# Kernel optimization log

Measured on AMD Instinct MI355X. Metric: run time of the kernel, lower is better.

## Reference

```python
import jax, jax.numpy as jnp
import numpy as np

HEADS = 4
DIM_HEAD = 32
GROUPS = 32  # min(256//4, 32)
EPS = 1e-5


def setup_inputs() -> dict:
    key = jax.random.key(0)
    ks = jax.random.split(key, 5)
    B, C, H, W = 16, 256, 64, 64
    CD, HC, WC = 512, 32, 32
    hid = HEADS * DIM_HEAD  # 128
    return {
        "x": jax.random.normal(ks[0], (B, C, H, W), jnp.float32),
        "cond": jax.random.normal(ks[1], (B, CD, HC, WC), jnp.float32),
        "gn_w": jnp.ones((C,), jnp.float32),
        "gn_b": jnp.zeros((C,), jnp.float32),
        "w_q": jax.random.normal(ks[2], (hid, C), jnp.float32) * 0.05,
        "b_q": jnp.zeros((hid,), jnp.float32),
        "w_kv": jax.random.normal(ks[3], (2 * hid, CD), jnp.float32) * 0.05,
        "b_kv": jnp.zeros((2 * hid,), jnp.float32),
        "w_out": jax.random.normal(ks[4], (C, hid), jnp.float32) * 0.05,
        "b_out": jnp.zeros((C,), jnp.float32),
    }


def _group_norm(x, w, b):
    # x: (B, C, H, W); normalize per group over (channels-in-group, H, W)
    B, C, H, W = x.shape
    xg = x.reshape(B, GROUPS, C // GROUPS, H, W)
    mu = jnp.mean(xg, axis=(2, 3, 4), keepdims=True)
    var = jnp.var(xg, axis=(2, 3, 4), keepdims=True)
    xn = ((xg - mu) * jax.lax.rsqrt(var + EPS)).reshape(B, C, H, W)
    return xn * w[None, :, None, None] + b[None, :, None, None]


def _conv1x1(x, w, b):
    # x: (B, Cin, H, W), w: (Cout, Cin), b: (Cout,)
    return jnp.einsum('oc,bchw->bohw', w, x) + b[None, :, None, None]


def reference(x, cond, gn_w, gn_b, w_q, b_q, w_kv, b_kv, w_out, b_out):
    B, C, H, W = x.shape
    hid = HEADS * DIM_HEAD
    xn = _group_norm(x, gn_w, gn_b)
    q = _conv1x1(xn, w_q, b_q)          # (B, hid, H, W)
    kv = _conv1x1(cond, w_kv, b_kv)     # (B, 2*hid, Hc, Wc)
    Nc = kv.shape[2] * kv.shape[3]
    N = H * W
    k = kv[:, :hid].reshape(B, HEADS, DIM_HEAD, Nc)
    v = kv[:, hid:].reshape(B, HEADS, DIM_HEAD, Nc)
    q = q.reshape(B, HEADS, DIM_HEAD, N)
    k = jax.nn.softmax(k, axis=-1)
    # kv outer product: (B, heads, d, e)
    context = jnp.einsum('bhdn,bhen->bhde', k, v)
    # query contraction over d: (B, heads, e, n)
    out = jnp.einsum('bhde,bhdn->bhen', context, q)
    out = out.reshape(B, hid, H, W)
    return _conv1x1(out, w_out, b_out)
```

## Files before the change

### kernel.cpp

```cpp
#include <hip/hip_runtime.h>
#include <hip/hip_bf16.h>

typedef __attribute__((ext_vector_type(8))) short bf16x8;
typedef __attribute__((ext_vector_type(4))) float f32x4;

__device__ __forceinline__ ushort f2bf(float f) {
    __hip_bfloat16 h = __float2bfloat16(f);
    return __builtin_bit_cast(ushort, h);
}
__device__ __forceinline__ float bflo(unsigned u) { return __uint_as_float(u << 16); }
__device__ __forceinline__ float bfhi(unsigned u) { return __uint_as_float(u & 0xffff0000u); }

__device__ __forceinline__ void unpack8(uint4 r, float* o) {
    o[0] = bflo(r.x); o[1] = bfhi(r.x); o[2] = bflo(r.y); o[3] = bfhi(r.y);
    o[4] = bflo(r.z); o[5] = bfhi(r.z); o[6] = bflo(r.w); o[7] = bfhi(r.w);
}

__global__ __launch_bounds__(256) void prep_kernel(const float* __restrict__ w,
                                                   ushort* __restrict__ o,
                                                   float* __restrict__ zbase,
                                                   const float* __restrict__ x,
                                                   float* __restrict__ statacc) {
    __shared__ float red[8];
    int bid = blockIdx.x, t = threadIdx.x;
    if (bid < 512) {
        int i = bid * 256 + t;
        if (i < 67584) zbase[i] = 0.f;
        o[i] = f2bf(w[i]);
    } else {
        int bg = bid - 512;
        const float4* xp = (const float4*)(x + (size_t)bg * 32768);
        float s = 0.f, ss = 0.f;
        #pragma unroll
        for (int j = 0; j < 32; ++j) {
            float4 v = xp[t + 256 * j];
            s  += v.x + v.y + v.z + v.w;
            ss += v.x*v.x + v.y*v.y + v.z*v.z + v.w*v.w;
        }
        #pragma unroll
        for (int off = 32; off > 0; off >>= 1) {
            s  += __shfl_down(s, off, 64);
            ss += __shfl_down(ss, off, 64);
        }
        int wave = t >> 6;
        if ((t & 63) == 0) { red[wave * 2] = s; red[wave * 2 + 1] = ss; }
        __syncthreads();
        if (t == 0) {
            statacc[bg * 2]     = red[0] + red[2] + red[4] + red[6];
            statacc[bg * 2 + 1] = red[1] + red[3] + red[5] + red[7];
        }
    }
}

__global__ __launch_bounds__(256) void kv_gemm(const ushort* __restrict__ wkv16,
                                               const float* __restrict__ cond,
                                               const float* __restrict__ b_kv,
                                               ushort* __restrict__ kv16) {
    __shared__ ushort lA[128 * 64];
    __shared__ ushort lB[64 * 64];
    __shared__ float scratch[64 * 64];
    int nb = blockIdx.x, ob = blockIdx.y, b = blockIdx.z;
    int col0 = nb * 64, row0 = ob * 128;
    int t = threadIdx.x;
    int l = t & 63, wid = t >> 6;
    int wr = wid >> 1, wc = wid & 1;
    int lr = l & 15, lg = l >> 4;
    const ushort* Ab = wkv16 + (size_t)row0 * 512;
    const float* Bb = cond + (size_t)b * 512 * 1024 + col0;
    int sp = t & 31, sj = t >> 5;
    int rA_ = t >> 3;
    int gA_ = (t & 7) ^ (rA_ & 7);
    int rB = t >> 4, gB = t & 15;
    uint4 a0_, a1_, a2_, a3_;
    float4 b0_, b1_, b2_, b3_;
    float4 c0_, c1_, c2_, c3_;
#define KG_LOADA(k0) { \
    a0_ = *(const uint4*)(Ab + (size_t)(rA_)      * 512 + (k0) + gA_ * 8); \
    a1_ = *(const uint4*)(Ab + (size_t)(32 + rA_) * 512 + (k0) + gA_ * 8); \
    a2_ = *(const uint4*)(Ab + (size_t)(64 + rA_) * 512 + (k0) + gA_ * 8); \
    a3_ = *(const uint4*)(Ab + (size_t)(96 + rA_) * 512 + (k0) + gA_ * 8); }
#define KG_LOADB0(k0) { \
    b0_ = *(const float4*)&Bb[(size_t)((k0) + rB)      * 1024 + gB * 4]; \
    b1_ = *(const float4*)&Bb[(size_t)((k0) + 16 + rB) * 1024 + gB * 4]; \
    b2_ = *(const float4*)&Bb[(size_t)((k0) + 32 + rB) * 1024 + gB * 4]; \
    b3_ = *(const float4*)&Bb[(size_t)((k0) + 48 + rB) * 1024 + gB * 4]; }
#define KG_LOADB1(k0) { \
    c0_ = *(const float4*)&Bb[(size_t)((k0) + rB)      * 1024 + gB * 4]; \
    c1_ = *(const float4*)&Bb[(size_t)((k0) + 16 + rB) * 1024 + gB * 4]; \
    c2_ = *(const float4*)&Bb[(size_t)((k0) + 32 + rB) * 1024 + gB * 4]; \
    c3_ = *(const float4*)&Bb[(size_t)((k0) + 48 + rB) * 1024 + gB * 4]; }
#define KG_WRITEA() { \
    *(uint4*)((char*)lA + (size_t)(t) * 16)       = a0_; \
    *(uint4*)((char*)lA + (size_t)(256 + t) * 16) = a1_; \
    *(uint4*)((char*)lA + (size_t)(512 + t) * 16) = a2_; \
    *(uint4*)((char*)lA + (size_t)(768 + t) * 16) = a3_; }
#define KG_WRITEB(v0, v1, v2, v3) { \
    *(float4*)((char*)scratch + (rB)      * 256 + (gB ^ (((rB)      >> 1) & 15)) * 16) = v0; \
    *(float4*)((char*)scratch + (16 + rB) * 256 + (gB ^ (((16 + rB) >> 1) & 15)) * 16) = v1; \
    *(float4*)((char*)scratch + (32 + rB) * 256 + (gB ^ (((32 + rB) >> 1) & 15)) * 16) = v2; \
    *(float4*)((char*)scratch + (48 + rB) * 256 + (gB ^ (((48 + rB) >> 1) & 15)) * 16) = v3; }
#define KG_PACK() { \
    int swz = sp & 15; \
    float4 s0 = *(const float4*)((char*)scratch + (2*sp)   * 256 + ((2*sj)   ^ swz) * 16); \
    float4 s1 = *(const float4*)((char*)scratch + (2*sp)   * 256 + ((2*sj+1) ^ swz) * 16); \
    float4 s2 = *(const float4*)((char*)scratch + (2*sp+1) * 256 + ((2*sj)   ^ swz) * 16); \
    float4 s3 = *(const float4*)((char*)scratch + (2*sp+1) * 256 + ((2*sj+1) ^ swz) * 16); \
    float c0v[8] = {s0.x, s0.y, s0.z, s0.w, s1.x, s1.y, s1.z, s1.w}; \
    float c1v[8] = {s2.x, s2.y, s2.z, s2.w, s3.x, s3.y, s3.z, s3.w}; \
    _Pragma("unroll") \
    for (int w = 0; w < 8; ++w) { \
        int n = sj * 8 + w; \
        unsigned pk = (unsigned)f2bf(c0v[w]) | ((unsigned)f2bf(c1v[w]) << 16); \
        *(unsigned*)((char*)lB + n * 128 + (((sp >> 2) ^ (n & 7)) * 16) + (sp & 3) * 4) = pk; \
    } }
#define KG_MFMA() { \
    _Pragma("unroll") \
    for (int ks = 0; ks < 2; ++ks) { \
        bf16x8 av[4], bv[2]; \
        _Pragma("unroll") \
        for (int mi = 0; mi < 4; ++mi) { \
            int ar = wr * 64 + mi * 16 + lr; \
            int q = (ks * 4 + lg) ^ (ar & 7); \
            av[mi] = *(const bf16x8*)((const char*)lA + ar * 128 + q * 16); \
        } \
        _Pragma("unroll") \
        for (int ni = 0; ni < 2; ++ni) { \
            int br = wc * 32 + ni * 16 + lr; \
            int q = (ks * 4 + lg) ^ (br & 7); \
            bv[ni] = *(const bf16x8*)((const char*)lB + br * 128 + q * 16); \
        } \
        _Pragma("unroll") \
        for (int mi = 0; mi < 4; ++mi) \
            _Pragma("unroll") \
            for (int ni = 0; ni < 2; ++ni) \
                acc[mi][ni] = __builtin_amdgcn_mfma_f32_16x16x32_bf16( \
                    av[mi], bv[ni], acc[mi][ni], 0, 0, 0); \
    } }
    KG_LOADA(0); KG_LOADB0(0); KG_LOADB1(64);
    f32x4 acc[4][2] = {};
    #pragma unroll
    for (int ii = 0; ii < 4; ++ii) {
        int k0 = ii * 128;
        KG_WRITEA();
        KG_WRITEB(b0_, b1_, b2_, b3_);
        __syncthreads();
        KG_LOADA(k0 + 64);
        if (ii < 3) KG_LOADB0(k0 + 128);
        KG_PACK();
        __syncthreads();
        KG_MFMA();
        __syncthreads();
        KG_WRITEA();
        KG_WRITEB(c0_, c1_, c2_, c3_);
        __syncthreads();
        if (ii < 3) { KG_LOADA(k0 + 128); KG_LOADB1(k0 + 192); }
        KG_PACK();
        __syncthreads();
        KG_MFMA();
        __syncthreads();
    }
#undef KG_LOADA
#undef KG_LOADB0
#undef KG_LOADB1
#undef KG_WRITEA
#undef KG_WRITEB
#undef KG_PACK
#undef KG_MFMA
    int orow = row0 + wr * 64, ocol = col0 + wc * 32 + lr;
    #pragma unroll
    for (int mi = 0; mi < 4; ++mi) {
        int rb = orow + mi * 16 + lg * 4;
        float4 b4 = *(const float4*)&b_kv[rb];
        float bvr[4] = {b4.x, b4.y, b4.z, b4.w};
        #pragma unroll
        for (int ni = 0; ni < 2; ++ni) {
            int cc = ocol + ni * 16;
            #pragma unroll
            for (int r = 0; r < 4; ++r)
                kv16[((size_t)b * 256 + rb + r) * 1024 + cc] = f2bf(acc[mi][ni][r] + bvr[r]);
        }
    }
}

__global__ __launch_bounds__(256) void ctx_partial_kernel(const ushort* __restrict__ kv,
                                                          float* __restrict__ rowsum,
                                                          float* __restrict__ ctx) {
    int bh = blockIdx.y, b = bh >> 2, h = bh & 3;
    int n0 = blockIdx.x * 128;
    __shared__ float pl[32][129], vl[32][129];
    int t = threadIdx.x;
    int r = t >> 3, cs = (t & 7) * 16;
    const ushort* kp = kv + ((size_t)b * 256 + h * 32 + r) * 1024 + n0 + cs;
    const ushort* vp = kv + ((size_t)b * 256 + 128 + h * 32 + r) * 1024 + n0 + cs;
    float kvals[16], vvals[16];
    unpack8(((const uint4*)kp)[0], kvals);
    unpack8(((const uint4*)kp)[1], kvals + 8);
    unpack8(((const uint4*)vp)[0], vvals);
    unpack8(((const uint4*)vp)[1], vvals + 8);
    float psum = 0.f;
    #pragma unroll
    for (int i = 0; i < 16; ++i) {
        float e = __expf(kvals[i]);
        pl[r][cs + i] = e;
        vl[r][cs + i] = vvals[i];
        psum += e;
    }
    psum += __shfl_xor(psum, 1, 64);
    psum += __shfl_xor(psum, 2, 64);
    psum += __shfl_xor(psum, 4, 64);
    if ((t & 7) == 0) atomicAdd(&rowsum[bh * 32 + r], psum);
    __syncthreads();
    int d0 = t >> 5, e0 = t & 31;
    float acc[4] = {0.f, 0.f, 0.f, 0.f};
    #pragma unroll 8
    for (int nn = 0; nn < 128; ++nn) {
        float vv = vl[e0][nn];
        #pragma unroll
        for (int i = 0; i < 4; ++i)
            acc[i] += pl[d0 + 8 * i][nn] * vv;
    }
    #pragma unroll
    for (int i = 0; i < 4; ++i)
        atomicAdd(&ctx[((size_t)bh * 32 + d0 + 8 * i) * 32 + e0], acc[i]);
}

__global__ __launch_bounds__(256) void a_kernel(const float* __restrict__ ctx,
                                                const float* __restrict__ rowsum,
                                                const float* __restrict__ w_out,
                                                const float* __restrict__ w_q,
                                                const float* __restrict__ b_q,
                                                const float* __restrict__ statacc,
                                                const float* __restrict__ gn_w,
                                                const float* __restrict__ gn_b,
                                                const float* __restrict__ b_out,
                                                ushort* __restrict__ A16,
                                                float* __restrict__ biasb) {
    __shared__ float ctxl[4][32][33];
    __shared__ float wol[16][128];
    __shared__ float ml[16][128];
    __shared__ float cbuf[256][17];
    __shared__ float pbuf[16][17];
    int b = blockIdx.x >> 4, ot = (blockIdx.x & 15) << 4;
    int t = threadIdx.x;
    #pragma unroll
    for (int j = 0; j < 16; ++j) {
        int e = t + 256 * j;
        float inv = 1.f / rowsum[b * 128 + (e >> 5)];
        ctxl[e >> 10][(e >> 5) & 31][e & 31] = ctx[(size_t)b * 4096 + e] * inv;
    }
    #pragma unroll
    for (int j = 0; j < 8; ++j) {
        int e = t + 256 * j;
        wol[e >> 7][e & 127] = w_out[(ot + (e >> 7)) * 128 + (e & 127)];
    }
    __syncthreads();
    #pragma unroll
    for (int j = 0; j < 8; ++j) {
        int e = t + 256 * j;
        int o = e >> 7, hd = e & 127, h = hd >> 5, d = hd & 31;
        float acc = 0.f;
        #pragma unroll
        for (int ee = 0; ee < 32; ++ee) acc += wol[o][h * 32 + ee] * ctxl[h][d][ee];
        ml[o][hd] = acc;
    }
    __syncthreads();
    int c = t, g = c >> 3;
    float a0 = statacc[(b * 32 + g) * 2], a1 = statacc[(b * 32 + g) * 2 + 1];
    float mu  = a0 * (1.f / 32768.f);
    float var = a1 * (1.f / 32768.f) - mu * mu;
    float sc = rsqrtf(var + 1e-5f) * gn_w[c];
    float tc = gn_b[c] - mu * sc;
    float wt[16];
    #pragma unroll
    for (int o = 0; o < 16; ++o) wt[o] = 0.f;
    for (int hd = 0; hd < 128; ++hd) {
        float wq = w_q[hd * 256 + c];
        #pragma unroll
        for (int o = 0; o < 16; ++o) wt[o] += ml[o][hd] * wq;
    }
    ushort* Abp = A16 + ((size_t)b * 256 + ot) * 256 + c;
    #pragma unroll
    for (int o = 0; o < 16; ++o) {
        Abp[(size_t)o * 256] = f2bf(wt[o] * sc);
        cbuf[c][o] = wt[o] * tc;
    }
    __syncthreads();
    {
        int o = t >> 4, seg = t & 15;
        float p = 0.f;
        #pragma unroll
        for (int i = 0; i < 16; ++i) p += cbuf[seg * 16 + i][o];
        pbuf[o][seg] = p;
    }
    __syncthreads();
    if (t < 16) {
        int o = t;
        float sum = 0.f;
        #pragma unroll
        for (int s2 = 0; s2 < 16; ++s2) sum += pbuf[o][s2];
        float md = 0.f;
        #pragma unroll 8
        for (int hd = 0; hd < 128; ++hd) md += ml[o][hd] * b_q[hd];
        biasb[(size_t)b * 256 + ot + o] = sum + md + b_out[ot + o];
    }
}

__global__ __launch_bounds__(512) void out_gemm_fused(const ushort* __restrict__ A16,
                                                      const float* __restrict__ x,
                                                      const float* __restrict__ biasb,
                                                      float* __restrict__ out) {
    __shared__ ushort lA[256 * 64];
    __shared__ ushort lB[128 * 64];
    __shared__ float scratch[64 * 128];
    int b = blockIdx.y;
    int n0 = blockIdx.x * 128;
    int t = threadIdx.x;
    int l = t & 63, wid = t >> 6;
    int wr = wid >> 1, wc = wid & 1;
    int lr = l & 15, lg = l >> 4;
    const ushort* Ab = A16 + (size_t)b * 65536;
    const float* xb = x + (size_t)b * 256 * 4096 + n0;
    int sp = t & 31, sj = t >> 5;
    uint4 a0_, a1_, a2_, a3_;
    float4 b0_, b1_, b2_, b3_;
    int rA = t >> 3, gA = (t & 7) ^ (rA & 7);
    int rB = t >> 5, gB = t & 31;
#define OG_LOADA(k0) { \
    a0_ = *(const uint4*)(Ab + (size_t)(rA)       * 256 + (k0) + gA * 8); \
    a1_ = *(const uint4*)(Ab + (size_t)(64 + rA)  * 256 + (k0) + gA * 8); \
    a2_ = *(const uint4*)(Ab + (size_t)(128 + rA) * 256 + (k0) + gA * 8); \
    a3_ = *(const uint4*)(Ab + (size_t)(192 + rA) * 256 + (k0) + gA * 8); }
#define OG_LOADB(k0) { \
    b0_ = *(const float4*)&xb[(size_t)((k0) + rB)      * 4096 + gB * 4]; \
    b1_ = *(const float4*)&xb[(size_t)((k0) + 16 + rB) * 4096 + gB * 4]; \
    b2_ = *(const float4*)&xb[(size_t)((k0) + 32 + rB) * 4096 + gB * 4]; \
    b3_ = *(const float4*)&xb[(size_t)((k0) + 48 + rB) * 4096 + gB * 4]; }
    OG_LOADA(0); OG_LOADB(0);
    f32x4 acc[4][4] = {};
    for (int it = 0; it < 4; ++it) {
        *(uint4*)((char*)lA + (size_t)t * 16)          = a0_;
        *(uint4*)((char*)lA + (size_t)(512 + t) * 16)  = a1_;
        *(uint4*)((char*)lA + (size_t)(1024 + t) * 16) = a2_;
        *(uint4*)((char*)lA + (size_t)(1536 + t) * 16) = a3_;
        *(float4*)((char*)scratch + (rB)      * 512 + (gB ^ (((rB)      >> 1) & 31)) * 16) = b0_;
        *(float4*)((char*)scratch + (16 + rB) * 512 + (gB ^ (((16 + rB) >> 1) & 31)) * 16) = b1_;
        *(float4*)((char*)scratch + (32 + rB) * 512 + (gB ^ (((32 + rB) >> 1) & 31)) * 16) = b2_;
        *(float4*)((char*)scratch + (48 + rB) * 512 + (gB ^ (((48 + rB) >> 1) & 31)) * 16) = b3_;
        __syncthreads();
        if (it < 3) { OG_LOADA(it * 64 + 64); OG_LOADB(it * 64 + 64); }
        {
            int swz = sp & 31;
            float4 s0 = *(const float4*)((char*)scratch + (2*sp)   * 512 + ((2*sj)   ^ swz) * 16);
            float4 s1 = *(const float4*)((char*)scratch + (2*sp)   * 512 + ((2*sj+1) ^ swz) * 16);
            float4 s2 = *(const float4*)((char*)scratch + (2*sp+1) * 512 + ((2*sj)   ^ swz) * 16);
            float4 s3 = *(const float4*)((char*)scratch + (2*sp+1) * 512 + ((2*sj+1) ^ swz) * 16);
            float c0v[8] = {s0.x, s0.y, s0.z, s0.w, s1.x, s1.y, s1.z, s1.w};
            float c1v[8] = {s2.x, s2.y, s2.z, s2.w, s3.x, s3.y, s3.z, s3.w};
            #pragma unroll
            for (int w = 0; w < 8; ++w) {
                int n = sj * 8 + w;
                unsigned pk = (unsigned)f2bf(c0v[w]) | ((unsigned)f2bf(c1v[w]) << 16);
                *(unsigned*)((char*)lB + n * 128 + (((sp >> 2) ^ (n & 7)) * 16) + (sp & 3) * 4) = pk;
            }
        }
        __syncthreads();
        #pragma unroll
        for (int ks = 0; ks < 2; ++ks) {
            bf16x8 av[4], bv[4];
            #pragma unroll
            for (int mi = 0; mi < 4; ++mi) {
                int ar = wr * 64 + mi * 16 + lr;
                int q = (ks * 4 + lg) ^ (ar & 7);
                av[mi] = *(const bf16x8*)((const char*)lA + ar * 128 + q * 16);
            }
            #pragma unroll
            for (int ni = 0; ni < 4; ++ni) {
                int br = wc * 64 + ni * 16 + lr;
                int q = (ks * 4 + lg) ^ (br & 7);
                bv[ni] = *(const bf16x8*)((const char*)lB + br * 128 + q * 16);
            }
            #pragma unroll
            for (int mi = 0; mi < 4; ++mi)
                #pragma unroll
                for (int ni = 0; ni < 4; ++ni)
                    acc[mi][ni] = __builtin_amdgcn_mfma_f32_16x16x32_bf16(
                        av[mi], bv[ni], acc[mi][ni], 0, 0, 0);
        }
        __syncthreads();
    }
#undef OG_LOADA
#undef OG_LOADB
    const float* bp = biasb + (size_t)b * 256;
    int orow = wr * 64, ocol = n0 + wc * 64 + lr;
    #pragma unroll
    for (int mi = 0; mi < 4; ++mi) {
        int rb = orow + mi * 16 + lg * 4;
        float4 b4 = *(const float4*)&bp[rb];
        float bvr[4] = {b4.x, b4.y, b4.z, b4.w};
        #pragma unroll
        for (int ni = 0; ni < 4; ++ni) {
            int cc = ocol + ni * 16;
            #pragma unroll
            for (int r = 0; r < 4; ++r)
                out[((size_t)b * 256 + rb + r) * 4096 + cc] = acc[mi][ni][r] + bvr[r];
        }
    }
}

extern "C" void kernel_launch(void* const* d_in, const int* in_sizes, int n_in,
                              void* d_out, int out_size, void* d_ws, size_t ws_size,
                              hipStream_t stream) {
    const float* x     = (const float*)d_in[0];
    const float* cond  = (const float*)d_in[1];
    const float* gn_w  = (const float*)d_in[2];
    const float* gn_b  = (const float*)d_in[3];
    const float* w_q   = (const float*)d_in[4];
    const float* b_q   = (const float*)d_in[5];
    const float* w_kv  = (const float*)d_in[6];
    const float* b_kv  = (const float*)d_in[7];
    const float* w_out = (const float*)d_in[8];
    const float* b_out = (const float*)d_in[9];
    float* out = (float*)d_out;

    float* f       = (float*)d_ws;
    float* statacc = f;
    float* rowsum  = f + 1024;
    float* ctx     = f + 3072;
    float* biasb   = f + 68608;
    ushort* u      = (ushort*)(f + 72704);
    ushort* wkv16  = u;
    ushort* kv16   = u + 131072;
    ushort* A16    = u + 4325376;

    prep_kernel<<<1024, 256, 0, stream>>>(w_kv, wkv16, rowsum, x, statacc);
    kv_gemm<<<dim3(16, 2, 16), 256, 0, stream>>>(wkv16, cond, b_kv, kv16);
    ctx_partial_kernel<<<dim3(8, 64), 256, 0, stream>>>(kv16, rowsum, ctx);
    a_kernel<<<256, 256, 0, stream>>>(ctx, rowsum, w_out, w_q, b_q, statacc,
                                      gn_w, gn_b, b_out, A16, biasb);
    out_gemm_fused<<<dim3(32, 16), 512, 0, stream>>>(A16, x, biasb, out);
}
```

Baseline: 84.10 us.

## Fuse kv GEMM with weight conversion and groupnorm stats into one kernel

Merges the prep kernel, which converted w_kv to bf16, zeroed the workspace and computed groupnorm statistics, into the kv GEMM launch. Blocks 0-511 now run the kv GEMM and convert fp32 weights to bf16 on the fly while staging them into LDS. Blocks 512-1023 do the statistics and zeroing. This removes one launch, the wkv16 round trip through memory, and lets the stats reduction run alongside the GEMM. In exchange it drops the double-buffered B prefetch, uses a single-stage loop, and loads A at twice the bytes because it is fp32, with the weight conversion repeated in every block.

```diff
diff --git a/kernel.cpp b/kernel.cpp
--- a/kernel.cpp
+++ b/kernel.cpp
@@ -8,6 +8,9 @@
     __hip_bfloat16 h = __float2bfloat16(f);
     return __builtin_bit_cast(ushort, h);
 }
+__device__ __forceinline__ unsigned pack2(float a, float b) {
+    return (unsigned)f2bf(a) | ((unsigned)f2bf(b) << 16);
+}
 __device__ __forceinline__ float bflo(unsigned u) { return __uint_as_float(u << 16); }
 __device__ __forceinline__ float bfhi(unsigned u) { return __uint_as_float(u & 0xffff0000u); }
 
@@ -16,90 +19,65 @@
     o[4] = bflo(r.z); o[5] = bfhi(r.z); o[6] = bflo(r.w); o[7] = bfhi(r.w);
 }
 
-__global__ __launch_bounds__(256) void prep_kernel(const float* __restrict__ w,
-                                                   ushort* __restrict__ o,
-                                                   float* __restrict__ zbase,
-                                                   const float* __restrict__ x,
-                                                   float* __restrict__ statacc) {
+__global__ __launch_bounds__(256) void kvprep_kernel(const float* __restrict__ w_kv,
+                                                     const float* __restrict__ cond,
+                                                     const float* __restrict__ b_kv,
+                                                     ushort* __restrict__ kv16,
+                                                     const float* __restrict__ x,
+                                                     float* __restrict__ statacc,
+                                                     float* __restrict__ zbase) {
+    __shared__ ushort lA[128 * 64];
+    __shared__ ushort lB[64 * 64];
+    __shared__ float scratch[64 * 64];
     __shared__ float red[8];
     int bid = blockIdx.x, t = threadIdx.x;
     if (bid < 512) {
-        int i = bid * 256 + t;
-        if (i < 67584) zbase[i] = 0.f;
-        o[i] = f2bf(w[i]);
-    } else {
-        int bg = bid - 512;
-        const float4* xp = (const float4*)(x + (size_t)bg * 32768);
-        float s = 0.f, ss = 0.f;
-        #pragma unroll
-        for (int j = 0; j < 32; ++j) {
-            float4 v = xp[t + 256 * j];
-            s  += v.x + v.y + v.z + v.w;
-            ss += v.x*v.x + v.y*v.y + v.z*v.z + v.w*v.w;
-        }
-        #pragma unroll
-        for (int off = 32; off > 0; off >>= 1) {
-            s  += __shfl_down(s, off, 64);
-            ss += __shfl_down(ss, off, 64);
-        }
-        int wave = t >> 6;
-        if ((t & 63) == 0) { red[wave * 2] = s; red[wave * 2 + 1] = ss; }
-        __syncthreads();
-        if (t == 0) {
-            statacc[bg * 2]     = red[0] + red[2] + red[4] + red[6];
-            statacc[bg * 2 + 1] = red[1] + red[3] + red[5] + red[7];
-        }
-    }
-}
-
-__global__ __launch_bounds__(256) void kv_gemm(const ushort* __restrict__ wkv16,
-                                               const float* __restrict__ cond,
-                                               const float* __restrict__ b_kv,
-                                               ushort* __restrict__ kv16) {
-    __shared__ ushort lA[128 * 64];
-    __shared__ ushort lB[64 * 64];
-    __shared__ float scratch[64 * 64];
-    int nb = blockIdx.x, ob = blockIdx.y, b = blockIdx.z;
-    int col0 = nb * 64, row0 = ob * 128;
-    int t = threadIdx.x;
-    int l = t & 63, wid = t >> 6;
-    int wr = wid >> 1, wc = wid & 1;
-    int lr = l & 15, lg = l >> 4;
-    const ushort* Ab = wkv16 + (size_t)row0 * 512;
-    const float* Bb = cond + (size_t)b * 512 * 1024 + col0;
-    int sp = t & 31, sj = t >> 5;
-    int rA_ = t >> 3;
-    int gA_ = (t & 7) ^ (rA_ & 7);
-    int rB = t >> 4, gB = t & 15;
-    uint4 a0_, a1_, a2_, a3_;
-    float4 b0_, b1_, b2_, b3_;
-    float4 c0_, c1_, c2_, c3_;
-#define KG_LOADA(k0) { \
-    a0_ = *(const uint4*)(Ab + (size_t)(rA_)      * 512 + (k0) + gA_ * 8); \
-    a1_ = *(const uint4*)(Ab + (size_t)(32 + rA_) * 512 + (k0) + gA_ * 8); \
-    a2_ = *(const uint4*)(Ab + (size_t)(64 + rA_) * 512 + (k0) + gA_ * 8); \
-    a3_ = *(const uint4*)(Ab + (size_t)(96 + rA_) * 512 + (k0) + gA_ * 8); }
-#define KG_LOADB0(k0) { \
-    b0_ = *(const float4*)&Bb[(size_t)((k0) + rB)      * 1024 + gB * 4]; \
-    b1_ = *(const float4*)&Bb[(size_t)((k0) + 16 + rB) * 1024 + gB * 4]; \
-    b2_ = *(const float4*)&Bb[(size_t)((k0) + 32 + rB) * 1024 + gB * 4]; \
-    b3_ = *(const float4*)&Bb[(size_t)((k0) + 48 + rB) * 1024 + gB * 4]; }
-#define KG_LOADB1(k0) { \
-    c0_ = *(const float4*)&Bb[(size_t)((k0) + rB)      * 1024 + gB * 4]; \
-    c1_ = *(const float4*)&Bb[(size_t)((k0) + 16 + rB) * 1024 + gB * 4]; \
-    c2_ = *(const float4*)&Bb[(size_t)((k0) + 32 + rB) * 1024 + gB * 4]; \
-    c3_ = *(const float4*)&Bb[(size_t)((k0) + 48 + rB) * 1024 + gB * 4]; }
-#define KG_WRITEA() { \
-    *(uint4*)((char*)lA + (size_t)(t) * 16)       = a0_; \
-    *(uint4*)((char*)lA + (size_t)(256 + t) * 16) = a1_; \
-    *(uint4*)((char*)lA + (size_t)(512 + t) * 16) = a2_; \
-    *(uint4*)((char*)lA + (size_t)(768 + t) * 16) = a3_; }
-#define KG_WRITEB(v0, v1, v2, v3) { \
-    *(float4*)((char*)scratch + (rB)      * 256 + (gB ^ (((rB)      >> 1) & 15)) * 16) = v0; \
-    *(float4*)((char*)scratch + (16 + rB) * 256 + (gB ^ (((16 + rB) >> 1) & 15)) * 16) = v1; \
-    *(float4*)((char*)scratch + (32 + rB) * 256 + (gB ^ (((32 + rB) >> 1) & 15)) * 16) = v2; \
-    *(float4*)((char*)scratch + (48 + rB) * 256 + (gB ^ (((48 + rB) >> 1) & 15)) * 16) = v3; }
-#define KG_PACK() { \
+        int nb = bid & 15, ob = (bid >> 4) & 1, b = bid >> 5;
+        int col0 = nb * 64, row0 = ob * 128;
+        int l = t & 63, wid = t >> 6;
+        int wr = wid >> 1, wc = wid & 1;
+        int lr = l & 15, lg = l >> 4;
+        const float* Ab32 = w_kv + (size_t)row0 * 512;
+        const float* Bb = cond + (size_t)b * 512 * 1024 + col0;
+        int sp = t & 31, sj = t >> 5;
+        int rA = t >> 3, gAr = t & 7, gw = gAr ^ (rA & 7);
+        int rB = t >> 4, gB = t & 15;
+        float4 ka0_, ka1_, ka2_, ka3_, ka4_, ka5_, ka6_, ka7_;
+        float4 kb0_, kb1_, kb2_, kb3_;
+#define KP_LOADA(k0) { \
+    ka0_ = *(const float4*)&Ab32[(size_t)(rA)      * 512 + (k0) + gAr * 8]; \
+    ka1_ = *(const float4*)&Ab32[(size_t)(rA)      * 512 + (k0) + gAr * 8 + 4]; \
+    ka2_ = *(const float4*)&Ab32[(size_t)(32 + rA) * 512 + (k0) + gAr * 8]; \
+    ka3_ = *(const float4*)&Ab32[(size_t)(32 + rA) * 512 + (k0) + gAr * 8 + 4]; \
+    ka4_ = *(const float4*)&Ab32[(size_t)(64 + rA) * 512 + (k0) + gAr * 8]; \
+    ka5_ = *(const float4*)&Ab32[(size_t)(64 + rA) * 512 + (k0) + gAr * 8 + 4]; \
+    ka6_ = *(const float4*)&Ab32[(size_t)(96 + rA) * 512 + (k0) + gAr * 8]; \
+    ka7_ = *(const float4*)&Ab32[(size_t)(96 + rA) * 512 + (k0) + gAr * 8 + 4]; }
+#define KP_LOADB(k0) { \
+    kb0_ = *(const float4*)&Bb[(size_t)((k0) + rB)      * 1024 + gB * 4]; \
+    kb1_ = *(const float4*)&Bb[(size_t)((k0) + 16 + rB) * 1024 + gB * 4]; \
+    kb2_ = *(const float4*)&Bb[(size_t)((k0) + 32 + rB) * 1024 + gB * 4]; \
+    kb3_ = *(const float4*)&Bb[(size_t)((k0) + 48 + rB) * 1024 + gB * 4]; }
+#define KP_WRITEA() { \
+    uint4 p; \
+    p.x = pack2(ka0_.x, ka0_.y); p.y = pack2(ka0_.z, ka0_.w); \
+    p.z = pack2(ka1_.x, ka1_.y); p.w = pack2(ka1_.z, ka1_.w); \
+    *(uint4*)((char*)lA + (size_t)((rA)      * 8 + gw) * 16) = p; \
+    p.x = pack2(ka2_.x, ka2_.y); p.y = pack2(ka2_.z, ka2_.w); \
+    p.z = pack2(ka3_.x, ka3_.y); p.w = pack2(ka3_.z, ka3_.w); \
+    *(uint4*)((char*)lA + (size_t)((32 + rA) * 8 + gw) * 16) = p; \
+    p.x = pack2(ka4_.x, ka4_.y); p.y = pack2(ka4_.z, ka4_.w); \
+    p.z = pack2(ka5_.x, ka5_.y); p.w = pack2(ka5_.z, ka5_.w); \
+    *(uint4*)((char*)lA + (size_t)((64 + rA) * 8 + gw) * 16) = p; \
+    p.x = pack2(ka6_.x, ka6_.y); p.y = pack2(ka6_.z, ka6_.w); \
+    p.z = pack2(ka7_.x, ka7_.y); p.w = pack2(ka7_.z, ka7_.w); \
+    *(uint4*)((char*)lA + (size_t)((96 + rA) * 8 + gw) * 16) = p; }
+#define KP_WRITEB() { \
+    *(float4*)((char*)scratch + (rB)      * 256 + (gB ^ (((rB)      >> 1) & 15)) * 16) = kb0_; \
+    *(float4*)((char*)scratch + (16 + rB) * 256 + (gB ^ (((16 + rB) >> 1) & 15)) * 16) = kb1_; \
+    *(float4*)((char*)scratch + (32 + rB) * 256 + (gB ^ (((32 + rB) >> 1) & 15)) * 16) = kb2_; \
+    *(float4*)((char*)scratch + (48 + rB) * 256 + (gB ^ (((48 + rB) >> 1) & 15)) * 16) = kb3_; }
+#define KP_PACKB() { \
     int swz = sp & 15; \
     float4 s0 = *(const float4*)((char*)scratch + (2*sp)   * 256 + ((2*sj)   ^ swz) * 16); \
     float4 s1 = *(const float4*)((char*)scratch + (2*sp)   * 256 + ((2*sj+1) ^ swz) * 16); \
@@ -110,74 +88,84 @@
     _Pragma("unroll") \
     for (int w = 0; w < 8; ++w) { \
         int n = sj * 8 + w; \
-        unsigned pk = (unsigned)f2bf(c0v[w]) | ((unsigned)f2bf(c1v[w]) << 16); \
+        unsigned pk = pack2(c0v[w], c1v[w]); \
         *(unsigned*)((char*)lB + n * 128 + (((sp >> 2) ^ (n & 7)) * 16) + (sp & 3) * 4) = pk; \
     } }
-#define KG_MFMA() { \
-    _Pragma("unroll") \
-    for (int ks = 0; ks < 2; ++ks) { \
-        bf16x8 av[4], bv[2]; \
-        _Pragma("unroll") \
-        for (int mi = 0; mi < 4; ++mi) { \
-            int ar = wr * 64 + mi * 16 + lr; \
-            int q = (ks * 4 + lg) ^ (ar & 7); \
-            av[mi] = *(const bf16x8*)((const char*)lA + ar * 128 + q * 16); \
-        } \
-        _Pragma("unroll") \
-        for (int ni = 0; ni < 2; ++ni) { \
-            int br = wc * 32 + ni * 16 + lr; \
-            int q = (ks * 4 + lg) ^ (br & 7); \
-            bv[ni] = *(const bf16x8*)((const char*)lB + br * 128 + q * 16); \
-        } \
-        _Pragma("unroll") \
-        for (int mi = 0; mi < 4; ++mi) \
-            _Pragma("unroll") \
-            for (int ni = 0; ni < 2; ++ni) \
-                acc[mi][ni] = __builtin_amdgcn_mfma_f32_16x16x32_bf16( \
-                    av[mi], bv[ni], acc[mi][ni], 0, 0, 0); \
-    } }
-    KG_LOADA(0); KG_LOADB0(0); KG_LOADB1(64);
-    f32x4 acc[4][2] = {};
-    #pragma unroll
-    for (int ii = 0; ii < 4; ++ii) {
-        int k0 = ii * 128;
-        KG_WRITEA();
-        KG_WRITEB(b0_, b1_, b2_, b3_);
+        KP_LOADA(0); KP_LOADB(0);
+        f32x4 acc[4][2] = {};
+        for (int it = 0; it < 8; ++it) {
+            KP_WRITEA();
+            KP_WRITEB();
+            __syncthreads();
+            if (it < 7) { KP_LOADA(it * 64 + 64); KP_LOADB(it * 64 + 64); }
+            KP_PACKB();
+            __syncthreads();
+            #pragma unroll
+            for (int ks = 0; ks < 2; ++ks) {
+                bf16x8 av[4], bv[2];
+                #pragma unroll
+                for (int mi = 0; mi < 4; ++mi) {
+                    int ar = wr * 64 + mi * 16 + lr;
+                    int q = (ks * 4 + lg) ^ (ar & 7);
+                    av[mi] = *(const bf16x8*)((const char*)lA + ar * 128 + q * 16);
+                }
+                #pragma unroll
+                for (int ni = 0; ni < 2; ++ni) {
+                    int br = wc * 32 + ni * 16 + lr;
+                    int q = (ks * 4 + lg) ^ (br & 7);
+                    bv[ni] = *(const bf16x8*)((const char*)lB + br * 128 + q * 16);
+                }
+                #pragma unroll
+                for (int mi = 0; mi < 4; ++mi)
+                    #pragma unroll
+                    for (int ni = 0; ni < 2; ++ni)
+                        acc[mi][ni] = __builtin_amdgcn_mfma_f32_16x16x32_bf16(
+                            av[mi], bv[ni], acc[mi][ni], 0, 0, 0);
+            }
+            __syncthreads();
+        }
+#undef KP_LOADA
+#undef KP_LOADB
+#undef KP_WRITEA
+#undef KP_WRITEB
+#undef KP_PACKB
+        int orow = row0 + wr * 64, ocol = col0 + wc * 32 + lr;
+        #pragma unroll
+        for (int mi = 0; mi < 4; ++mi) {
+            int rb = orow + mi * 16 + lg * 4;
+            float4 b4 = *(const float4*)&b_kv[rb];
+            float bvr[4] = {b4.x, b4.y, b4.z, b4.w};
+            #pragma unroll
+            for (int ni = 0; ni < 2; ++ni) {
+                int cc = ocol + ni * 16;
+                #pragma unroll
+                for (int r = 0; r < 4; ++r)
+                    kv16[((size_t)b * 256 + rb + r) * 1024 + cc] = f2bf(acc[mi][ni][r] + bvr[r]);
+            }
+        }
+    } else {
+        int bg = bid - 512;
+        int zi = bg * 256 + t;
+        if (zi < 67584) zbase[zi] = 0.f;
+        const float4* xp = (const float4*)(x + (size_t)bg * 32768);
+        float s = 0.f, ss = 0.f;
+        #pragma unroll
+        for (int j = 0; j < 32; ++j) {
+            float4 v = xp[t + 256 * j];
+            s  += v.x + v.y + v.z + v.w;
+            ss += v.x*v.x + v.y*v.y + v.z*v.z + v.w*v.w;
+        }
+        #pragma unroll
+        for (int off = 32; off > 0; off >>= 1) {
+            s  += __shfl_down(s, off, 64);
+            ss += __shfl_down(ss, off, 64);
+        }
+        int wave = t >> 6;
+        if ((t & 63) == 0) { red[wave * 2] = s; red[wave * 2 + 1] = ss; }
         __syncthreads();
-        KG_LOADA(k0 + 64);
-        if (ii < 3) KG_LOADB0(k0 + 128);
-        KG_PACK();
-        __syncthreads();
-        KG_MFMA();
-        __syncthreads();
-        KG_WRITEA();
-        KG_WRITEB(c0_, c1_, c2_, c3_);
-        __syncthreads();
-        if (ii < 3) { KG_LOADA(k0 + 128); KG_LOADB1(k0 + 192); }
-        KG_PACK();
-        __syncthreads();
-        KG_MFMA();
-        __syncthreads();
-    }
-#undef KG_LOADA
-#undef KG_LOADB0
-#undef KG_LOADB1
-#undef KG_WRITEA
-#undef KG_WRITEB
-#undef KG_PACK
-#undef KG_MFMA
-    int orow = row0 + wr * 64, ocol = col0 + wc * 32 + lr;
-    #pragma unroll
-    for (int mi = 0; mi < 4; ++mi) {
-        int rb = orow + mi * 16 + lg * 4;
-        float4 b4 = *(const float4*)&b_kv[rb];
-        float bvr[4] = {b4.x, b4.y, b4.z, b4.w};
-        #pragma unroll
-        for (int ni = 0; ni < 2; ++ni) {
-            int cc = ocol + ni * 16;
-            #pragma unroll
-            for (int r = 0; r < 4; ++r)
-                kv16[((size_t)b * 256 + rb + r) * 1024 + cc] = f2bf(acc[mi][ni][r] + bvr[r]);
+        if (t == 0) {
+            statacc[bg * 2]     = red[0] + red[2] + red[4] + red[6];
+            statacc[bg * 2 + 1] = red[1] + red[3] + red[5] + red[7];
         }
     }
 }
@@ -359,7 +347,7 @@
             #pragma unroll
             for (int w = 0; w < 8; ++w) {
                 int n = sj * 8 + w;
-                unsigned pk = (unsigned)f2bf(c0v[w]) | ((unsigned)f2bf(c1v[w]) << 16);
+                unsigned pk = pack2(c0v[w], c1v[w]);
                 *(unsigned*)((char*)lB + n * 128 + (((sp >> 2) ^ (n & 7)) * 16) + (sp & 3) * 4) = pk;
             }
         }
@@ -428,12 +416,10 @@
     float* ctx     = f + 3072;
     float* biasb   = f + 68608;
     ushort* u      = (ushort*)(f + 72704);
-    ushort* wkv16  = u;
-    ushort* kv16   = u + 131072;
-    ushort* A16    = u + 4325376;
-
-    prep_kernel<<<1024, 256, 0, stream>>>(w_kv, wkv16, rowsum, x, statacc);
-    kv_gemm<<<dim3(16, 2, 16), 256, 0, stream>>>(wkv16, cond, b_kv, kv16);
+    ushort* kv16   = u;
+    ushort* A16    = u + 4194304;
+
+    kvprep_kernel<<<1024, 256, 0, stream>>>(w_kv, cond, b_kv, kv16, x, statacc, rowsum);
     ctx_partial_kernel<<<dim3(8, 64), 256, 0, stream>>>(kv16, rowsum, ctx);
     a_kernel<<<256, 256, 0, stream>>>(ctx, rowsum, w_out, w_q, b_q, statacc,
                                       gn_w, gn_b, b_out, A16, biasb);
```

Measured after the change: 80.67 us. 4.1% less time.
